# Optimization experiments

Hardware: AMD Instinct MI355X
Metric: run time of the kernel (lower is better)

Reference implementation:

```python
import jax, jax.numpy as jnp
import numpy as np

INPUT, HIDDEN, OUT = 30, 128, 11

def setup_inputs() -> dict:
    key = jax.random.key(0)
    ks = jax.random.split(key, 9)
    s_ih = 1.0 / np.sqrt(HIDDEN)
    def u(k, shape):
        return jax.random.uniform(k, shape, jnp.float32, -s_ih, s_ih)
    return {
        "x": jax.random.normal(ks[0], (4096, 256, INPUT), jnp.float32),
        "W_ih": u(ks[1], (4 * HIDDEN, INPUT)),
        "W_hh": u(ks[2], (4 * HIDDEN, HIDDEN)),
        "b_ih": u(ks[3], (4 * HIDDEN,)),
        "b_hh": u(ks[4], (4 * HIDDEN,)),
        "W0": u(ks[5], (HIDDEN, HIDDEN)),
        "b0": u(ks[6], (HIDDEN,)),
        "W1": u(ks[7], (OUT, HIDDEN)),
        "b1": u(ks[8], (OUT,)),
    }

def lstm_last_h(x, W_ih, W_hh, b_ih, b_hh):
    # x: [B, T, I]; precompute input projections for all timesteps
    B = x.shape[0]
    xg = jnp.einsum('bti,gi->btg', x, W_ih) + b_ih + b_hh  # [B, T, 4H]
    def step(carry, g_x):
        h, c = carry
        g = g_x + h @ W_hh.T  # [B, 4H]
        i, f, gg, o = jnp.split(g, 4, axis=-1)  # PyTorch gate order i,f,g,o
        i = jax.nn.sigmoid(i); f = jax.nn.sigmoid(f)
        gg = jnp.tanh(gg); o = jax.nn.sigmoid(o)
        c = f * c + i * gg
        h = o * jnp.tanh(c)
        return (h, c), None
    h0 = jnp.zeros((B, HIDDEN), x.dtype)
    c0 = jnp.zeros((B, HIDDEN), x.dtype)
    (h, c), _ = jax.lax.scan(step, (h0, c0), jnp.swapaxes(xg, 0, 1))
    return h

def reference(x, W_ih, W_hh, b_ih, b_hh, W0, b0, W1, b1):
    h = lstm_last_h(x, W_ih, W_hh, b_ih, b_hh)  # [B, H]
    y0 = jax.nn.relu(h @ W0.T + b0)
    return y0 @ W1.T + b1  # [B, 11]
```

## Files before the change

### kernel.cpp

```cpp
#include <hip/hip_runtime.h>

#define TT 256
#define II 30
#define HH 128
#define TB 16
#define AROW 168

typedef _Float16 half8 __attribute__((ext_vector_type(8)));
typedef float f32x4 __attribute__((ext_vector_type(4)));

#if __has_builtin(__builtin_amdgcn_exp2f)
#define EXP2(x) __builtin_amdgcn_exp2f(x)
#else
#define EXP2(x) exp2f(x)
#endif
#define RCP(x) __builtin_amdgcn_rcpf(x)

#define L2E 1.44269504089f
#define TWO_L2E 2.88539008177f

__device__ __forceinline__ float sig2(float a) {
  return RCP(1.0f + EXP2(-a));
}
__device__ __forceinline__ float tanh2(float a) {
  return fmaf(-2.0f, RCP(1.0f + EXP2(a)), 1.0f);
}
__device__ __forceinline__ float tanh2s(float c) {
  return tanh2(c * TWO_L2E);
}

__device__ __forceinline__ void lstm_step(
    int t, const _Float16* __restrict__ Ar, _Float16* __restrict__ Aw,
    const half8 (&bf)[4][5], const float (&bias)[4], float (&c)[4],
    float& xw, const float* __restrict__ xp, bool stg, int sS, int iS,
    int col, int grp, int w)
{
  float xn = 0.0f;
  if (stg && (t + 2 < TT)) xn = xp[(size_t)(t + 2) * II];

  half8 af[5];
  #pragma unroll
  for (int ks = 0; ks < 5; ++ks)
    af[ks] = *reinterpret_cast<const half8*>(&Ar[col * AROW + ks * 32 + grp * 8]);

  f32x4 a0 = {bias[0], bias[0], bias[0], bias[0]};
  f32x4 a1 = {bias[1], bias[1], bias[1], bias[1]};
  #pragma unroll
  for (int ks = 0; ks < 5; ++ks)
    a0 = __builtin_amdgcn_mfma_f32_16x16x32_f16(af[ks], bf[0][ks], a0, 0, 0, 0);
  #pragma unroll
  for (int ks = 0; ks < 5; ++ks)
    a1 = __builtin_amdgcn_mfma_f32_16x16x32_f16(af[ks], bf[1][ks], a1, 0, 0, 0);

  float ig[4], fg[4];
  #pragma unroll
  for (int r = 0; r < 4; ++r) { ig[r] = sig2(a0[r]); fg[r] = sig2(a1[r]); }

  f32x4 a2 = {bias[2], bias[2], bias[2], bias[2]};
  f32x4 a3 = {bias[3], bias[3], bias[3], bias[3]};
  #pragma unroll
  for (int ks = 0; ks < 5; ++ks)
    a2 = __builtin_amdgcn_mfma_f32_16x16x32_f16(af[ks], bf[2][ks], a2, 0, 0, 0);
  #pragma unroll
  for (int ks = 0; ks < 5; ++ks)
    a3 = __builtin_amdgcn_mfma_f32_16x16x32_f16(af[ks], bf[3][ks], a3, 0, 0, 0);

  #pragma unroll
  for (int r = 0; r < 4; ++r) {
    const float tg = tanh2(a2[r]);
    const float og = sig2(a3[r]);
    const float cn = fmaf(fg[r], c[r], ig[r] * tg);
    c[r] = cn;
    const float th = tanh2s(cn);
    Aw[(grp * 4 + r) * AROW + w * 16 + col] = (_Float16)(og * th);
  }

  if (stg && (t + 1 < TT)) Aw[sS * AROW + HH + iS] = (_Float16)xw;
  __syncthreads();
  xw = xn;
}

__global__ __launch_bounds__(512, 2)
void lstm_mfma(const float* __restrict__ x,
               const float* __restrict__ W_ih,
               const float* __restrict__ W_hh,
               const float* __restrict__ b_ih,
               const float* __restrict__ b_hh,
               const float* __restrict__ W0,
               const float* __restrict__ b0v,
               const float* __restrict__ W1,
               const float* __restrict__ b1v,
               float* __restrict__ out)
{
  __shared__ __align__(16) _Float16 Ab[2][TB * AROW];
  __shared__ float y0ls[TB * 132];

  const int tid = threadIdx.x;
  const int bbase = blockIdx.x * TB;
  const int w = tid >> 6;
  const int lane = tid & 63;
  const int col = lane & 15;
  const int grp = lane >> 4;

  half8 bf[4][5];
  float bias[4];
  #pragma unroll
  for (int g = 0; g < 4; ++g) {
    const float sc = (g == 2) ? TWO_L2E : L2E;
    const int n = g * 128 + w * 16 + col;
    #pragma unroll
    for (int ks = 0; ks < 4; ++ks) {
      const float4 p = *reinterpret_cast<const float4*>(W_hh + n * HH + ks * 32 + grp * 8);
      const float4 q = *reinterpret_cast<const float4*>(W_hh + n * HH + ks * 32 + grp * 8 + 4);
      bf[g][ks] = (half8){(_Float16)(p.x * sc), (_Float16)(p.y * sc),
                          (_Float16)(p.z * sc), (_Float16)(p.w * sc),
                          (_Float16)(q.x * sc), (_Float16)(q.y * sc),
                          (_Float16)(q.z * sc), (_Float16)(q.w * sc)};
    }
    {
      float v[8];
      #pragma unroll
      for (int j = 0; j < 8; ++j) {
        const int cc = grp * 8 + j;
        v[j] = (cc < II) ? W_ih[n * II + cc] * sc : 0.0f;
      }
      bf[g][4] = (half8){(_Float16)v[0], (_Float16)v[1], (_Float16)v[2], (_Float16)v[3],
                         (_Float16)v[4], (_Float16)v[5], (_Float16)v[6], (_Float16)v[7]};
    }
    bias[g] = (b_ih[n] + b_hh[n]) * sc;
  }

  const bool stg = (lane < 60);
  const int sS = w * 2 + (lane >= 30 ? 1 : 0);
  const int iS = lane % 30;
  const float* xp = x + (size_t)(bbase + sS) * (TT * II) + iS;
  float xa = 0.0f, xw = 0.0f;
  if (stg) { xa = xp[0]; xw = xp[II]; }

  if (tid < 256) {
    const int s = tid >> 4, u8 = (tid & 15) * 8;
    *reinterpret_cast<half8*>(&Ab[0][s * AROW + u8]) = (half8){0,0,0,0,0,0,0,0};
  }
  if (tid < 32) {
    const int b = tid >> 4, s = tid & 15;
    Ab[b][s * AROW + 158] = (_Float16)0.0f;
    Ab[b][s * AROW + 159] = (_Float16)0.0f;
  }
  if (stg) Ab[0][sS * AROW + HH + iS] = (_Float16)xa;

  float c[4] = {0.0f, 0.0f, 0.0f, 0.0f};
  __syncthreads();

  for (int t = 0; t < TT; t += 2) {
    lstm_step(t,     Ab[0], Ab[1], bf, bias, c, xw, xp, stg, sS, iS, col, grp, w);
    lstm_step(t + 1, Ab[1], Ab[0], bf, bias, c, xw, xp, stg, sS, iS, col, grp, w);
  }

  if (tid < 256) {
    const int s = tid >> 4;
    const int n0 = (tid & 15) * 8;
    float acch[8];
    #pragma unroll
    for (int nj = 0; nj < 8; ++nj) acch[nj] = b0v[n0 + nj];
    #pragma unroll
    for (int kb = 0; kb < 16; ++kb) {
      const half8 hh = *reinterpret_cast<const half8*>(&Ab[0][s * AROW + kb * 8]);
      float hf[8];
      #pragma unroll
      for (int j = 0; j < 8; ++j) hf[j] = (float)hh[j];
      #pragma unroll
      for (int nj = 0; nj < 8; ++nj) {
        const float4 w0 = *reinterpret_cast<const float4*>(W0 + (n0 + nj) * HH + kb * 8);
        const float4 w1 = *reinterpret_cast<const float4*>(W0 + (n0 + nj) * HH + kb * 8 + 4);
        acch[nj] = fmaf(hf[0], w0.x, fmaf(hf[1], w0.y, fmaf(hf[2], w0.z, fmaf(hf[3], w0.w,
                   fmaf(hf[4], w1.x, fmaf(hf[5], w1.y, fmaf(hf[6], w1.z, fmaf(hf[7], w1.w,
                        acch[nj]))))))));
      }
    }
    #pragma unroll
    for (int nj = 0; nj < 8; ++nj)
      y0ls[s * 132 + n0 + nj] = fmaxf(acch[nj], 0.0f);
  }
  __syncthreads();

  if (tid < TB * 11) {
    const int s = tid / 11;
    const int oo = tid % 11;
    float acc1 = b1v[oo];
    const float4* y4 = reinterpret_cast<const float4*>(y0ls + s * 132);
    const float4* w4 = reinterpret_cast<const float4*>(W1 + oo * HH);
    #pragma unroll 8
    for (int k4 = 0; k4 < 32; ++k4) {
      const float4 yv = y4[k4];
      const float4 wv4 = w4[k4];
      acc1 = fmaf(yv.x, wv4.x, fmaf(yv.y, wv4.y, fmaf(yv.z, wv4.z, fmaf(yv.w, wv4.w, acc1))));
    }
    out[(size_t)(bbase + s) * 11 + oo] = acc1;
  }
}

extern "C" void kernel_launch(void* const* d_in, const int* in_sizes, int n_in,
                              void* d_out, int out_size, void* d_ws, size_t ws_size,
                              hipStream_t stream) {
  const float* x    = (const float*)d_in[0];
  const float* W_ih = (const float*)d_in[1];
  const float* W_hh = (const float*)d_in[2];
  const float* b_ih = (const float*)d_in[3];
  const float* b_hh = (const float*)d_in[4];
  const float* W0   = (const float*)d_in[5];
  const float* b0   = (const float*)d_in[6];
  const float* W1   = (const float*)d_in[7];
  const float* b1   = (const float*)d_in[8];
  float* out = (float*)d_out;
  lstm_mfma<<<256, 512, 0, stream>>>(x, W_ih, W_hh, b_ih, b_hh, W0, b0, W1, b1, out);
}
```

Measured before the change: 278.0 us.

## Stage x in double-buffered 16-timestep LDS panels with vectorized loads

Replaces the per-timestep scalar global load of x (one float per lane, two steps ahead) with float4 loads of a 16-timestep window per sequence, converted to fp16 and written into a double-buffered LDS panel halfway through the current window. The hidden state and input parts of the MFMA A operand now live in separate LDS buffers. The aim is to cut the global-load latency and instruction count on the recurrent critical path. The cost is extra LDS and more registers for the staged window.

```diff
diff --git a/kernel.cpp b/kernel.cpp
--- a/kernel.cpp
+++ b/kernel.cpp
@@ -4,9 +4,13 @@
 #define II 30
 #define HH 128
 #define TB 16
-#define AROW 168
+#define HROWF 136
+#define XROWF 40
+#define XTT 16
+#define XPANEL (XTT * TB * XROWF)
 
 typedef _Float16 half8 __attribute__((ext_vector_type(8)));
+typedef _Float16 half2v __attribute__((ext_vector_type(2)));
 typedef float f32x4 __attribute__((ext_vector_type(4)));
 
 #if __has_builtin(__builtin_amdgcn_exp2f)
@@ -27,57 +31,6 @@
 }
 __device__ __forceinline__ float tanh2s(float c) {
   return tanh2(c * TWO_L2E);
-}
-
-__device__ __forceinline__ void lstm_step(
-    int t, const _Float16* __restrict__ Ar, _Float16* __restrict__ Aw,
-    const half8 (&bf)[4][5], const float (&bias)[4], float (&c)[4],
-    float& xw, const float* __restrict__ xp, bool stg, int sS, int iS,
-    int col, int grp, int w)
-{
-  float xn = 0.0f;
-  if (stg && (t + 2 < TT)) xn = xp[(size_t)(t + 2) * II];
-
-  half8 af[5];
-  #pragma unroll
-  for (int ks = 0; ks < 5; ++ks)
-    af[ks] = *reinterpret_cast<const half8*>(&Ar[col * AROW + ks * 32 + grp * 8]);
-
-  f32x4 a0 = {bias[0], bias[0], bias[0], bias[0]};
-  f32x4 a1 = {bias[1], bias[1], bias[1], bias[1]};
-  #pragma unroll
-  for (int ks = 0; ks < 5; ++ks)
-    a0 = __builtin_amdgcn_mfma_f32_16x16x32_f16(af[ks], bf[0][ks], a0, 0, 0, 0);
-  #pragma unroll
-  for (int ks = 0; ks < 5; ++ks)
-    a1 = __builtin_amdgcn_mfma_f32_16x16x32_f16(af[ks], bf[1][ks], a1, 0, 0, 0);
-
-  float ig[4], fg[4];
-  #pragma unroll
-  for (int r = 0; r < 4; ++r) { ig[r] = sig2(a0[r]); fg[r] = sig2(a1[r]); }
-
-  f32x4 a2 = {bias[2], bias[2], bias[2], bias[2]};
-  f32x4 a3 = {bias[3], bias[3], bias[3], bias[3]};
-  #pragma unroll
-  for (int ks = 0; ks < 5; ++ks)
-    a2 = __builtin_amdgcn_mfma_f32_16x16x32_f16(af[ks], bf[2][ks], a2, 0, 0, 0);
-  #pragma unroll
-  for (int ks = 0; ks < 5; ++ks)
-    a3 = __builtin_amdgcn_mfma_f32_16x16x32_f16(af[ks], bf[3][ks], a3, 0, 0, 0);
-
-  #pragma unroll
-  for (int r = 0; r < 4; ++r) {
-    const float tg = tanh2(a2[r]);
-    const float og = sig2(a3[r]);
-    const float cn = fmaf(fg[r], c[r], ig[r] * tg);
-    c[r] = cn;
-    const float th = tanh2s(cn);
-    Aw[(grp * 4 + r) * AROW + w * 16 + col] = (_Float16)(og * th);
-  }
-
-  if (stg && (t + 1 < TT)) Aw[sS * AROW + HH + iS] = (_Float16)xw;
-  __syncthreads();
-  xw = xn;
 }
 
 __global__ __launch_bounds__(512, 2)
@@ -92,12 +45,13 @@
                const float* __restrict__ b1v,
                float* __restrict__ out)
 {
-  __shared__ __align__(16) _Float16 Ab[2][TB * AROW];
+  __shared__ __align__(16) _Float16 Hb[2][TB * HROWF];
+  __shared__ __align__(16) _Float16 Xp[2][XPANEL];
   __shared__ float y0ls[TB * 132];
 
   const int tid = threadIdx.x;
   const int bbase = blockIdx.x * TB;
-  const int w = tid >> 6;
+  const int wv = tid >> 6;
   const int lane = tid & 63;
   const int col = lane & 15;
   const int grp = lane >> 4;
@@ -107,7 +61,7 @@
   #pragma unroll
   for (int g = 0; g < 4; ++g) {
     const float sc = (g == 2) ? TWO_L2E : L2E;
-    const int n = g * 128 + w * 16 + col;
+    const int n = g * 128 + wv * 16 + col;
     #pragma unroll
     for (int ks = 0; ks < 4; ++ks) {
       const float4 p = *reinterpret_cast<const float4*>(W_hh + n * HH + ks * 32 + grp * 8);
@@ -130,30 +84,105 @@
     bias[g] = (b_ih[n] + b_hh[n]) * sc;
   }
 
-  const bool stg = (lane < 60);
-  const int sS = w * 2 + (lane >= 30 ? 1 : 0);
-  const int iS = lane % 30;
-  const float* xp = x + (size_t)(bbase + sS) * (TT * II) + iS;
-  float xa = 0.0f, xw = 0.0f;
-  if (stg) { xa = xp[0]; xw = xp[II]; }
+  const bool stg = (tid < 480);
+  const int sS = stg ? (tid / 30) : 15;
+  const int qS = tid % 30;
+  const int g0 = qS * 16;
+  const int tt0 = g0 / 30;
+  const int i00 = g0 % 30;
+  const float* wbase = x + (size_t)(bbase + sS) * (TT * II);
+
+  float4 xr0, xr1, xr2, xr3;
+  auto xload = [&](int win) {
+    if (!stg) return;
+    const float* p = wbase + win * (XTT * II) + g0;
+    xr0 = *reinterpret_cast<const float4*>(p);
+    xr1 = *reinterpret_cast<const float4*>(p + 4);
+    xr2 = *reinterpret_cast<const float4*>(p + 8);
+    xr3 = *reinterpret_cast<const float4*>(p + 12);
+  };
+  auto xwrite = [&](int dstb) {
+    if (!stg) return;
+    _Float16* d = &Xp[dstb][0];
+    const float vv[16] = {xr0.x, xr0.y, xr0.z, xr0.w, xr1.x, xr1.y, xr1.z, xr1.w,
+                          xr2.x, xr2.y, xr2.z, xr2.w, xr3.x, xr3.y, xr3.z, xr3.w};
+    int tt = tt0, i = i00;
+    #pragma unroll
+    for (int j = 0; j < 16; ++j) {
+      d[tt * (TB * XROWF) + sS * XROWF + i] = (_Float16)vv[j];
+      ++i;
+      if (i == II) { i = 0; ++tt; }
+    }
+  };
 
   if (tid < 256) {
     const int s = tid >> 4, u8 = (tid & 15) * 8;
-    *reinterpret_cast<half8*>(&Ab[0][s * AROW + u8]) = (half8){0,0,0,0,0,0,0,0};
-  }
-  if (tid < 32) {
-    const int b = tid >> 4, s = tid & 15;
-    Ab[b][s * AROW + 158] = (_Float16)0.0f;
-    Ab[b][s * AROW + 159] = (_Float16)0.0f;
-  }
-  if (stg) Ab[0][sS * AROW + HH + iS] = (_Float16)xa;
+    *reinterpret_cast<half8*>(&Hb[0][s * HROWF + u8]) = (half8){0,0,0,0,0,0,0,0};
+  }
+  {
+    const int pb = tid >> 8, rr = tid & 255;
+    const int tt = rr >> 4, s = rr & 15;
+    *reinterpret_cast<half2v*>(&Xp[pb][tt * (TB * XROWF) + s * XROWF + II]) = (half2v){0, 0};
+  }
 
   float c[4] = {0.0f, 0.0f, 0.0f, 0.0f};
+
+  xload(0);
+  xwrite(0);
   __syncthreads();
 
-  for (int t = 0; t < TT; t += 2) {
-    lstm_step(t,     Ab[0], Ab[1], bf, bias, c, xw, xp, stg, sS, iS, col, grp, w);
-    lstm_step(t + 1, Ab[1], Ab[0], bf, bias, c, xw, xp, stg, sS, iS, col, grp, w);
+  auto step = [&](int tt_idx, const _Float16* Ar, _Float16* Aw, const _Float16* Xr) {
+    half8 af[5];
+    #pragma unroll
+    for (int ks = 0; ks < 4; ++ks)
+      af[ks] = *reinterpret_cast<const half8*>(&Ar[col * HROWF + ks * 32 + grp * 8]);
+    af[4] = *reinterpret_cast<const half8*>(&Xr[tt_idx * (TB * XROWF) + col * XROWF + grp * 8]);
+
+    f32x4 a0 = {bias[0], bias[0], bias[0], bias[0]};
+    f32x4 a1 = {bias[1], bias[1], bias[1], bias[1]};
+    #pragma unroll
+    for (int ks = 0; ks < 5; ++ks)
+      a0 = __builtin_amdgcn_mfma_f32_16x16x32_f16(af[ks], bf[0][ks], a0, 0, 0, 0);
+    #pragma unroll
+    for (int ks = 0; ks < 5; ++ks)
+      a1 = __builtin_amdgcn_mfma_f32_16x16x32_f16(af[ks], bf[1][ks], a1, 0, 0, 0);
+
+    float ig[4], fg[4];
+    #pragma unroll
+    for (int r = 0; r < 4; ++r) { ig[r] = sig2(a0[r]); fg[r] = sig2(a1[r]); }
+
+    f32x4 a2 = {bias[2], bias[2], bias[2], bias[2]};
+    f32x4 a3 = {bias[3], bias[3], bias[3], bias[3]};
+    #pragma unroll
+    for (int ks = 0; ks < 5; ++ks)
+      a2 = __builtin_amdgcn_mfma_f32_16x16x32_f16(af[ks], bf[2][ks], a2, 0, 0, 0);
+    #pragma unroll
+    for (int ks = 0; ks < 5; ++ks)
+      a3 = __builtin_amdgcn_mfma_f32_16x16x32_f16(af[ks], bf[3][ks], a3, 0, 0, 0);
+
+    #pragma unroll
+    for (int r = 0; r < 4; ++r) {
+      const float tg = tanh2(a2[r]);
+      const float og = sig2(a3[r]);
+      const float cn = fmaf(fg[r], c[r], ig[r] * tg);
+      c[r] = cn;
+      Aw[(grp * 4 + r) * HROWF + wv * 16 + col] = (_Float16)(og * tanh2s(cn));
+    }
+    __syncthreads();
+  };
+
+  for (int win = 0; win < 16; ++win) {
+    const _Float16* Xr = Xp[win & 1];
+    if (win + 1 < 16) xload(win + 1);
+    for (int k = 0; k < 8; k += 2) {
+      step(k,     Hb[0], Hb[1], Xr);
+      step(k + 1, Hb[1], Hb[0], Xr);
+    }
+    if (win + 1 < 16) xwrite((win + 1) & 1);
+    for (int k = 8; k < 16; k += 2) {
+      step(k,     Hb[0], Hb[1], Xr);
+      step(k + 1, Hb[1], Hb[0], Xr);
+    }
   }
 
   if (tid < 256) {
@@ -164,7 +193,7 @@
     for (int nj = 0; nj < 8; ++nj) acch[nj] = b0v[n0 + nj];
     #pragma unroll
     for (int kb = 0; kb < 16; ++kb) {
-      const half8 hh = *reinterpret_cast<const half8*>(&Ab[0][s * AROW + kb * 8]);
+      const half8 hh = *reinterpret_cast<const half8*>(&Hb[0][s * HROWF + kb * 8]);
       float hf[8];
       #pragma unroll
       for (int j = 0; j < 8; ++j) hf[j] = (float)hh[j];
```

After: 234.5 us. -15.6%, faster.
